# Performance work log

Hardware: AMD Instinct MI355X
Metric: run time of the kernel (lower is better)

The kernel has to match this reference:

```python
import jax, jax.numpy as jnp
import numpy as np

D_MODEL = 1024
N_HEADS = 16
HEAD_DIM = D_MODEL // N_HEADS  # 64
LATENT = 256
B, S = 2, 2048


def setup_inputs() -> dict:
    key = jax.random.key(0)
    ks = jax.random.split(key, 13)
    sc = 0.02
    inp = {
        'x': jax.random.normal(ks[0], (B, S, D_MODEL), jnp.float32),
        'Wq': jax.random.normal(ks[1], (D_MODEL, D_MODEL), jnp.float32) * sc,
        'bq': jnp.zeros((D_MODEL,), jnp.float32),
        'Wkd': jax.random.normal(ks[2], (D_MODEL, LATENT), jnp.float32) * sc,
        'bkd': jnp.zeros((LATENT,), jnp.float32),
        'Wvd': jax.random.normal(ks[3], (D_MODEL, LATENT), jnp.float32) * sc,
        'bvd': jnp.zeros((LATENT,), jnp.float32),
        'Wku': jax.random.normal(ks[4], (LATENT, D_MODEL), jnp.float32) * sc,
        'bku': jnp.zeros((D_MODEL,), jnp.float32),
        'Wvu': jax.random.normal(ks[5], (LATENT, D_MODEL), jnp.float32) * sc,
        'bvu': jnp.zeros((D_MODEL,), jnp.float32),
        'Wo': jax.random.normal(ks[6], (D_MODEL, D_MODEL), jnp.float32) * sc,
        'bo': jnp.zeros((D_MODEL,), jnp.float32),
    }
    return inp


def reference(x, Wq, bq, Wkd, bkd, Wvd, bvd, Wku, bku, Wvu, bvu, Wo, bo):
    b, s, _ = x.shape
    # projections
    Q = x @ Wq + bq                      # [b, s, d_model]
    K_latent = x @ Wkd + bkd             # [b, s, latent]
    V_latent = x @ Wvd + bvd             # [b, s, latent]
    K = K_latent @ Wku + bku             # [b, s, d_model]
    V = V_latent @ Wvu + bvu             # [b, s, d_model]
    # split heads
    Qh = Q.reshape(b, s, N_HEADS, HEAD_DIM)
    Kh = K.reshape(b, s, N_HEADS, HEAD_DIM)
    Vh = V.reshape(b, s, N_HEADS, HEAD_DIM)
    scale = 1.0 / jnp.sqrt(jnp.asarray(HEAD_DIM, x.dtype))
    scores = jnp.einsum('bqhd,bkhd->bhqk', Qh, Kh) * scale  # [b,h,s,s]
    attn = jax.nn.softmax(scores, axis=-1)
    ctx = jnp.einsum('bhqk,bkhd->bqhd', attn, Vh).reshape(b, s, D_MODEL)
    out = ctx @ Wo + bo
    return out
```

## Files before the change

### kernel.cpp

```cpp
#include <hip/hip_runtime.h>
#include <hip/hip_bf16.h>
#include <cstddef>

#define B_SZ 2
#define SEQ  2048
#define DM   1024
#define NH   16
#define HD   64
#define LAT  256
#define MTOT (B_SZ*SEQ)
#define NQKV 1536
#define QSCALE 0.18033688011112042f

typedef short bf16x8 __attribute__((ext_vector_type(8)));
typedef float floatx4 __attribute__((ext_vector_type(4)));
typedef float floatx16 __attribute__((ext_vector_type(16)));
typedef unsigned short u16;

#if __has_builtin(__builtin_amdgcn_exp2f)
#define EXP2(x) __builtin_amdgcn_exp2f(x)
#else
#define EXP2(x) exp2f(x)
#endif

__device__ __forceinline__ u16 f2bf(float f) {
  union { float f; unsigned u; } a; a.f = f;
  unsigned r = a.u + 0x7FFFu + ((a.u >> 16) & 1u);
  return (u16)(r >> 16);
}

__device__ __forceinline__ floatx4 mfma16(bf16x8 a, bf16x8 b, floatx4 c) {
  return __builtin_amdgcn_mfma_f32_16x16x32_bf16(a, b, c, 0, 0, 0);
}

__device__ __forceinline__ floatx16 mfma32(bf16x8 a, bf16x8 b, floatx16 c) {
  return __builtin_amdgcn_mfma_f32_32x32x16_bf16(a, b, c, 0, 0, 0);
}

__device__ __forceinline__ void load16(const u16* g, u16* l) {
  __builtin_amdgcn_global_load_lds((const __attribute__((address_space(1))) unsigned*)g,
                                   (__attribute__((address_space(3))) unsigned*)l, 16, 0, 0);
}

__device__ void transpose_tile(const float* __restrict__ W, u16* __restrict__ WT,
                               int K, int N, int k0, int n0, u16 (*t)[65]) {
  const int r = threadIdx.x >> 4;
  const int c4 = (threadIdx.x & 15) * 4;
#pragma unroll
  for (int s = 0; s < 4; s++) {
    int row = s * 16 + r;
    float4 v = *(const float4*)&W[(size_t)(k0 + row) * N + n0 + c4];
    t[row][c4 + 0] = f2bf(v.x); t[row][c4 + 1] = f2bf(v.y);
    t[row][c4 + 2] = f2bf(v.z); t[row][c4 + 3] = f2bf(v.w);
  }
  __syncthreads();
  const int r2 = threadIdx.x >> 2;
  const int c8 = (threadIdx.x & 3) * 16;
  __align__(16) u16 tmp[16];
#pragma unroll
  for (int i = 0; i < 16; i++) tmp[i] = t[c8 + i][r2];
  u16* dst = WT + (size_t)(n0 + r2) * K + k0 + c8;
  *(bf16x8*)dst       = *(const bf16x8*)&tmp[0];
  *(bf16x8*)(dst + 8) = *(const bf16x8*)&tmp[8];
}

__global__ __launch_bounds__(256)
void prep_k(const float* __restrict__ x, u16* __restrict__ xb,
            const float* __restrict__ Wq, const float* __restrict__ Wkd,
            const float* __restrict__ Wvd, const float* __restrict__ Wku,
            const float* __restrict__ Wvu, const float* __restrict__ Wo,
            u16* __restrict__ WstkT, u16* __restrict__ WkuT,
            u16* __restrict__ WvuT, u16* __restrict__ WoT,
            const float* __restrict__ bq, const float* __restrict__ bkd,
            const float* __restrict__ bvd, float* __restrict__ bqkv) {
  __shared__ u16 t[64][65];
  const int blk = blockIdx.x;
  if (blk < 4096) {
    int i = blk * 256 + threadIdx.x;
    float4 v = ((const float4*)x)[i];
    ushort4 o; o.x = f2bf(v.x); o.y = f2bf(v.y); o.z = f2bf(v.z); o.w = f2bf(v.w);
    ((ushort4*)xb)[i] = o;
  } else if (blk < 4352) {
    int tt = blk - 4096;
    transpose_tile(Wq, WstkT, DM, DM, (tt >> 4) * 64, (tt & 15) * 64, t);
  } else if (blk < 4416) {
    int tt = blk - 4352;
    transpose_tile(Wkd, WstkT + (size_t)DM * DM, DM, LAT, (tt >> 2) * 64, (tt & 3) * 64, t);
  } else if (blk < 4480) {
    int tt = blk - 4416;
    transpose_tile(Wvd, WstkT + (size_t)1280 * DM, DM, LAT, (tt >> 2) * 64, (tt & 3) * 64, t);
  } else if (blk < 4544) {
    int tt = blk - 4480;
    transpose_tile(Wku, WkuT, LAT, DM, (tt >> 4) * 64, (tt & 15) * 64, t);
  } else if (blk < 4608) {
    int tt = blk - 4544;
    transpose_tile(Wvu, WvuT, LAT, DM, (tt >> 4) * 64, (tt & 15) * 64, t);
  } else if (blk < 4864) {
    int tt = blk - 4608;
    transpose_tile(Wo, WoT, DM, DM, (tt >> 4) * 64, (tt & 15) * 64, t);
  } else {
    int i = (blk - 4864) * 256 + threadIdx.x;
    float v = (i < 1024) ? bq[i] : (i < 1280) ? bkd[i - 1024] : bvd[i - 1280];
    bqkv[i] = v;
  }
}

template<int TM, int OUT_BF16, int VT1>
__global__ __launch_bounds__(256)
void gemm_bt(const u16* __restrict__ A0, const u16* __restrict__ A1,
             const u16* __restrict__ BT0, const u16* __restrict__ BT1,
             const float* __restrict__ bias0, const float* __restrict__ bias1,
             void* __restrict__ C0, void* __restrict__ C1,
             int M, int N, int Kd, int lda, float qscale, int qcols) {
  constexpr int FM = TM / 32;
  __shared__ u16 As[TM * 64];
  __shared__ u16 Bs[64 * 64];
  const u16* A  = blockIdx.z ? A1 : A0;
  const u16* BT = blockIdx.z ? BT1 : BT0;
  const float* bias = blockIdx.z ? bias1 : bias0;
  void* C = blockIdx.z ? C1 : C0;

  const int tid = threadIdx.x;
  const int m0 = blockIdx.y * TM, n0 = blockIdx.x * 64;
  const int wave = tid >> 6, lane = tid & 63;
  const int l15 = lane & 15, quad = lane >> 4;
  const int wm = (wave >> 1) * (TM / 2), wn = (wave & 1) * 32;

  floatx4 acc[FM][2];
#pragma unroll
  for (int i = 0; i < FM; i++)
#pragma unroll
    for (int j = 0; j < 2; j++) acc[i][j] = (floatx4){0.f, 0.f, 0.f, 0.f};

  const int tr = tid >> 3;
  const int tc8 = (tid & 7) * 8;
  const u16* Ag = A  + (size_t)(m0 + tr) * lda + tc8;
  const u16* Bg = BT + (size_t)(n0 + tr) * Kd + tc8;
  u16* AsW = &As[(size_t)tid * 8];
  u16* BsW = &Bs[(size_t)tid * 8];

  for (int k0 = 0; k0 < Kd; k0 += 64) {
    __syncthreads();
#pragma unroll
    for (int s = 0; s < FM; s++)
      load16(Ag + (size_t)(s * 32) * lda + k0, AsW + s * 2048);
#pragma unroll
    for (int s = 0; s < 2; s++)
      load16(Bg + (size_t)(s * 32) * Kd  + k0, BsW + s * 2048);
    __syncthreads();
#pragma unroll
    for (int kk = 0; kk < 2; kk++) {
      bf16x8 af[FM], bfr[2];
#pragma unroll
      for (int i = 0; i < FM; i++)
        af[i]  = *(const bf16x8*)&As[(wm + i * 16 + l15) * 64 + kk * 32 + quad * 8];
#pragma unroll
      for (int j = 0; j < 2; j++)
        bfr[j] = *(const bf16x8*)&Bs[(wn + j * 16 + l15) * 64 + kk * 32 + quad * 8];
#pragma unroll
      for (int i = 0; i < FM; i++)
#pragma unroll
        for (int j = 0; j < 2; j++)
          acc[i][j] = mfma16(af[i], bfr[j], acc[i][j]);
    }
  }

  if (VT1 && blockIdx.z == 1) {
#pragma unroll
    for (int i = 0; i < FM; i++) {
      int row = m0 + wm + i * 16 + quad * 4;
      int bb = row >> 11, sb = row & 2047;
#pragma unroll
      for (int j = 0; j < 2; j++) {
        int col = n0 + wn + j * 16 + l15;
        float bv = bias[col];
        union { u16 u[4]; uint2 w2; } tv;
#pragma unroll
        for (int r = 0; r < 4; r++) tv.u[r] = f2bf(acc[i][j][r] + bv);
        *(uint2*)((u16*)C + ((size_t)(bb * 16 + (col >> 6)) * 64 + (col & 63)) * SEQ + sb) = tv.w2;
      }
    }
  } else {
#pragma unroll
    for (int i = 0; i < FM; i++) {
      int row = m0 + wm + i * 16 + quad * 4;
#pragma unroll
      for (int j = 0; j < 2; j++) {
        int col = n0 + wn + j * 16 + l15;
        float bv = bias[col];
        float sc = (col < qcols) ? qscale : 1.f;
#pragma unroll
        for (int r = 0; r < 4; r++) {
          float v = (acc[i][j][r] + bv) * sc;
          if (OUT_BF16) ((u16*)C)[(size_t)(row + r) * N + col] = f2bf(v);
          else          ((float*)C)[(size_t)(row + r) * N + col] = v;
        }
      }
    }
  }
}

__global__ __launch_bounds__(256, 3)
void attn_fused(const u16* __restrict__ Q, const u16* __restrict__ K,
                const u16* __restrict__ VT, u16* __restrict__ CTX) {
  __shared__ __align__(16) u16 KVt[2][2][64][64];
  const int lin = blockIdx.y * gridDim.x + blockIdx.x;
  const int idx = lin >> 3;
  const int bh = (lin & 7) * 4 + (idx >> 4);
  const int q0 = (idx & 15) * 128;
  const int b = bh >> 4, h = bh & 15;
  const int wave = threadIdx.x >> 6, lane = threadIdx.x & 63;
  const int l31 = lane & 31;
  const int hi = lane >> 5;
  const int lr = lane >> 3;
  const int cx = (lane & 7) ^ lr;

  bf16x8 qf[4];
  {
    const u16* Qp = Q + (size_t)(b * SEQ + q0 + wave * 32 + l31) * NQKV + h * HD + hi * 8;
#pragma unroll
    for (int dc = 0; dc < 4; dc++)
      qf[dc] = *(const bf16x8*)(Qp + dc * 16);
  }

  const u16* Ks[2];
  const u16* Vs[2];
#pragma unroll
  for (int s = 0; s < 2; s++) {
    int r = wave * 8 + s * 32 + lr;
    Ks[s] = K + (size_t)(b * SEQ + r) * DM + h * HD + cx * 8;
    Vs[s] = VT + ((size_t)bh * HD + r) * SEQ + cx * 8;
  }

  floatx16 o[2];
  const floatx16 zf16 = {0.f,0.f,0.f,0.f,0.f,0.f,0.f,0.f,0.f,0.f,0.f,0.f,0.f,0.f,0.f,0.f};
  o[0] = zf16; o[1] = zf16;
  float ls = 0.f;

#pragma unroll
  for (int s = 0; s < 2; s++) {
    load16(Ks[s], &KVt[0][0][wave * 8 + s * 32][0]);
    load16(Vs[s], &KVt[0][1][wave * 8 + s * 32][0]);
  }
  __syncthreads();

#pragma unroll 2
  for (int t = 0; t < 32; ++t) {
    const int cur = t & 1, nxt = cur ^ 1;
    if (t < 31) {
      const int kt = (t + 1) * 64;
#pragma unroll
      for (int s = 0; s < 2; s++) {
        load16(Ks[s] + (size_t)kt * DM, &KVt[nxt][0][wave * 8 + s * 32][0]);
        load16(Vs[s] + kt,              &KVt[nxt][1][wave * 8 + s * 32][0]);
      }
    }
#pragma unroll
    for (int kh = 0; kh < 2; kh++) {
      const int rk = kh * 32 + l31;
      bf16x8 kf[4];
#pragma unroll
      for (int dc = 0; dc < 4; dc++)
        kf[dc] = *(const bf16x8*)&KVt[cur][0][rk][((dc * 2 + hi) ^ (rk & 7)) * 8];
      floatx16 z = zf16;
      __builtin_amdgcn_s_setprio(1);
#pragma unroll
      for (int dc = 0; dc < 4; dc++) z = mfma32(kf[dc], qf[dc], z);
      __builtin_amdgcn_s_setprio(0);
      {
        float p0 = EXP2(z[0]), p1 = EXP2(z[1]), p2 = EXP2(z[2]), p3 = EXP2(z[3]);
        float p4 = EXP2(z[4]), p5 = EXP2(z[5]), p6 = EXP2(z[6]), p7 = EXP2(z[7]);
        ls += ((p0 + p1) + (p2 + p3)) + ((p4 + p5) + (p6 + p7));
        unsigned w0 = __builtin_amdgcn_perm(__float_as_uint(p1) + 0x8000u,
                                            __float_as_uint(p0) + 0x8000u, 0x07060302u);
        unsigned w1 = __builtin_amdgcn_perm(__float_as_uint(p3) + 0x8000u,
                                            __float_as_uint(p2) + 0x8000u, 0x07060302u);
        unsigned w2 = __builtin_amdgcn_perm(__float_as_uint(p5) + 0x8000u,
                                            __float_as_uint(p4) + 0x8000u, 0x07060302u);
        unsigned w3 = __builtin_amdgcn_perm(__float_as_uint(p7) + 0x8000u,
                                            __float_as_uint(p6) + 0x8000u, 0x07060302u);
        unsigned s0 = (unsigned)__shfl_xor((int)w0, 32);
        unsigned s1 = (unsigned)__shfl_xor((int)w1, 32);
        unsigned s2 = (unsigned)__shfl_xor((int)w2, 32);
        unsigned s3 = (unsigned)__shfl_xor((int)w3, 32);
        union { unsigned u[4]; bf16x8 v; } b0;
        b0.u[0] = hi ? s2 : w0;
        b0.u[1] = hi ? s3 : w1;
        b0.u[2] = hi ? w2 : s0;
        b0.u[3] = hi ? w3 : s1;
        bf16x8 vf0 = *(const bf16x8*)&KVt[cur][1][l31     ][((kh * 4 + hi) ^ (l31 & 7)) * 8];
        bf16x8 vf1 = *(const bf16x8*)&KVt[cur][1][32 + l31][((kh * 4 + hi) ^ (l31 & 7)) * 8];
        __builtin_amdgcn_s_setprio(1);
        o[0] = mfma32(vf0, b0.v, o[0]);
        o[1] = mfma32(vf1, b0.v, o[1]);
        __builtin_amdgcn_s_setprio(0);
      }
      {
        float p0 = EXP2(z[8]),  p1 = EXP2(z[9]),  p2 = EXP2(z[10]), p3 = EXP2(z[11]);
        float p4 = EXP2(z[12]), p5 = EXP2(z[13]), p6 = EXP2(z[14]), p7 = EXP2(z[15]);
        ls += ((p0 + p1) + (p2 + p3)) + ((p4 + p5) + (p6 + p7));
        unsigned w0 = __builtin_amdgcn_perm(__float_as_uint(p1) + 0x8000u,
                                            __float_as_uint(p0) + 0x8000u, 0x07060302u);
        unsigned w1 = __builtin_amdgcn_perm(__float_as_uint(p3) + 0x8000u,
                                            __float_as_uint(p2) + 0x8000u, 0x07060302u);
        unsigned w2 = __builtin_amdgcn_perm(__float_as_uint(p5) + 0x8000u,
                                            __float_as_uint(p4) + 0x8000u, 0x07060302u);
        unsigned w3 = __builtin_amdgcn_perm(__float_as_uint(p7) + 0x8000u,
                                            __float_as_uint(p6) + 0x8000u, 0x07060302u);
        unsigned s0 = (unsigned)__shfl_xor((int)w0, 32);
        unsigned s1 = (unsigned)__shfl_xor((int)w1, 32);
        unsigned s2 = (unsigned)__shfl_xor((int)w2, 32);
        unsigned s3 = (unsigned)__shfl_xor((int)w3, 32);
        union { unsigned u[4]; bf16x8 v; } b1;
        b1.u[0] = hi ? s2 : w0;
        b1.u[1] = hi ? s3 : w1;
        b1.u[2] = hi ? w2 : s0;
        b1.u[3] = hi ? w3 : s1;
        bf16x8 vf0 = *(const bf16x8*)&KVt[cur][1][l31     ][((kh * 4 + 2 + hi) ^ (l31 & 7)) * 8];
        bf16x8 vf1 = *(const bf16x8*)&KVt[cur][1][32 + l31][((kh * 4 + 2 + hi) ^ (l31 & 7)) * 8];
        __builtin_amdgcn_s_setprio(1);
        o[0] = mfma32(vf0, b1.v, o[0]);
        o[1] = mfma32(vf1, b1.v, o[1]);
        __builtin_amdgcn_s_setprio(0);
      }
    }
    __syncthreads();
  }

  const float lsum = ls + __shfl_xor(ls, 32);
  const float inv = 1.f / lsum;
  u16* Crow = CTX + (size_t)(b * SEQ + q0 + wave * 32 + l31) * DM + h * HD + hi * 4;
#pragma unroll
  for (int dh = 0; dh < 2; dh++)
#pragma unroll
    for (int g = 0; g < 4; g++) {
      union { u16 u[4]; uint2 w2; } tv;
#pragma unroll
      for (int r = 0; r < 4; r++)
        tv.u[r] = f2bf(o[dh][4 * g + r] * inv);
      *(uint2*)(Crow + dh * 32 + g * 8) = tv.w2;
    }
}

extern "C" void kernel_launch(void* const* d_in, const int* in_sizes, int n_in,
                              void* d_out, int out_size, void* d_ws, size_t ws_size,
                              hipStream_t stream) {
  const float* x   = (const float*)d_in[0];
  const float* Wq  = (const float*)d_in[1];
  const float* bq  = (const float*)d_in[2];
  const float* Wkd = (const float*)d_in[3];
  const float* bkd = (const float*)d_in[4];
  const float* Wvd = (const float*)d_in[5];
  const float* bvd = (const float*)d_in[6];
  const float* Wku = (const float*)d_in[7];
  const float* bku = (const float*)d_in[8];
  const float* Wvu = (const float*)d_in[9];
  const float* bvu = (const float*)d_in[10];
  const float* Wo  = (const float*)d_in[11];
  const float* bo  = (const float*)d_in[12];
  float* out = (float*)d_out;

  float* bqkv = (float*)d_ws;
  u16* p = (u16*)((char*)d_ws + 1536 * sizeof(float));
  u16* xb    = p; p += (size_t)MTOT * DM;
  u16* WstkT = p; p += (size_t)NQKV * DM;
  u16* WkuT  = p; p += (size_t)DM * LAT;
  u16* WvuT  = p; p += (size_t)DM * LAT;
  u16* WoT   = p; p += (size_t)DM * DM;
  u16* QKVb  = p; p += (size_t)MTOT * NQKV;
  u16* Kb    = p; p += (size_t)MTOT * DM;
  u16* VTb   = p; p += (size_t)MTOT * DM;
  u16* CXb   = p; p += (size_t)MTOT * DM;

  prep_k<<<4870, 256, 0, stream>>>(x, xb, Wq, Wkd, Wvd, Wku, Wvu, Wo,
                                   WstkT, WkuT, WvuT, WoT, bq, bkd, bvd, bqkv);

  gemm_bt<128, 1, 0><<<dim3(NQKV / 64, MTOT / 128, 1), 256, 0, stream>>>(
      xb, xb, WstkT, WstkT, bqkv, bqkv, QKVb, QKVb, MTOT, NQKV, DM, DM, QSCALE, DM);
  gemm_bt<128, 1, 1><<<dim3(DM / 64, MTOT / 128, 2), 256, 0, stream>>>(
      QKVb + 1024, QKVb + 1280, WkuT, WvuT, bku, bvu, Kb, VTb, MTOT, DM, LAT, NQKV, 1.f, 0);

  attn_fused<<<dim3(SEQ / 128, B_SZ * NH), 256, 0, stream>>>(QKVb, Kb, VTb, CXb);

  gemm_bt<64, 0, 0><<<dim3(DM / 64, MTOT / 64, 1), 256, 0, stream>>>(
      CXb, CXb, WoT, WoT, bo, bo, out, out, MTOT, DM, DM, DM, 1.f, 0);
}
```

Measured before the change: 205.5 us.

## Split key sequence across two wave groups per block in attention

Doubles the attention block to 512 threads, with two groups of four waves each handling half of the key/value sequence for the same 128 queries. Partial outputs and row sums are merged through shared memory at the end. This raises wave-level parallelism and latency hiding per CU. In exchange it doubles LDS use and adds a reduction step, and the tighter launch bound may cause register pressure or spills.

```diff
diff --git a/kernel.cpp b/kernel.cpp
--- a/kernel.cpp
+++ b/kernel.cpp
@@ -200,16 +200,18 @@
   }
 }
 
-__global__ __launch_bounds__(256, 3)
+__global__ __launch_bounds__(512, 3)
 void attn_fused(const u16* __restrict__ Q, const u16* __restrict__ K,
                 const u16* __restrict__ VT, u16* __restrict__ CTX) {
-  __shared__ __align__(16) u16 KVt[2][2][64][64];
+  __shared__ __align__(16) u16 KVt[2][2][2][64][64];
   const int lin = blockIdx.y * gridDim.x + blockIdx.x;
   const int idx = lin >> 3;
   const int bh = (lin & 7) * 4 + (idx >> 4);
   const int q0 = (idx & 15) * 128;
   const int b = bh >> 4, h = bh & 15;
   const int wave = threadIdx.x >> 6, lane = threadIdx.x & 63;
+  const int qw = wave & 3;
+  const int kw = wave >> 2;
   const int l31 = lane & 31;
   const int hi = lane >> 5;
   const int lr = lane >> 3;
@@ -217,7 +219,7 @@
 
   bf16x8 qf[4];
   {
-    const u16* Qp = Q + (size_t)(b * SEQ + q0 + wave * 32 + l31) * NQKV + h * HD + hi * 8;
+    const u16* Qp = Q + (size_t)(b * SEQ + q0 + qw * 32 + l31) * NQKV + h * HD + hi * 8;
 #pragma unroll
     for (int dc = 0; dc < 4; dc++)
       qf[dc] = *(const bf16x8*)(Qp + dc * 16);
@@ -227,9 +229,9 @@
   const u16* Vs[2];
 #pragma unroll
   for (int s = 0; s < 2; s++) {
-    int r = wave * 8 + s * 32 + lr;
-    Ks[s] = K + (size_t)(b * SEQ + r) * DM + h * HD + cx * 8;
-    Vs[s] = VT + ((size_t)bh * HD + r) * SEQ + cx * 8;
+    int r = qw * 8 + s * 32 + lr;
+    Ks[s] = K + (size_t)(b * SEQ + kw * 1024 + r) * DM + h * HD + cx * 8;
+    Vs[s] = VT + ((size_t)bh * HD + r) * SEQ + kw * 1024 + cx * 8;
   }
 
   floatx16 o[2];
@@ -239,20 +241,20 @@
 
 #pragma unroll
   for (int s = 0; s < 2; s++) {
-    load16(Ks[s], &KVt[0][0][wave * 8 + s * 32][0]);
-    load16(Vs[s], &KVt[0][1][wave * 8 + s * 32][0]);
+    load16(Ks[s], &KVt[kw][0][0][qw * 8 + s * 32][0]);
+    load16(Vs[s], &KVt[kw][0][1][qw * 8 + s * 32][0]);
   }
   __syncthreads();
 
 #pragma unroll 2
-  for (int t = 0; t < 32; ++t) {
+  for (int t = 0; t < 16; ++t) {
     const int cur = t & 1, nxt = cur ^ 1;
-    if (t < 31) {
+    if (t < 15) {
       const int kt = (t + 1) * 64;
 #pragma unroll
       for (int s = 0; s < 2; s++) {
-        load16(Ks[s] + (size_t)kt * DM, &KVt[nxt][0][wave * 8 + s * 32][0]);
-        load16(Vs[s] + kt,              &KVt[nxt][1][wave * 8 + s * 32][0]);
+        load16(Ks[s] + (size_t)kt * DM, &KVt[kw][nxt][0][qw * 8 + s * 32][0]);
+        load16(Vs[s] + kt,              &KVt[kw][nxt][1][qw * 8 + s * 32][0]);
       }
     }
 #pragma unroll
@@ -261,7 +263,7 @@
       bf16x8 kf[4];
 #pragma unroll
       for (int dc = 0; dc < 4; dc++)
-        kf[dc] = *(const bf16x8*)&KVt[cur][0][rk][((dc * 2 + hi) ^ (rk & 7)) * 8];
+        kf[dc] = *(const bf16x8*)&KVt[kw][cur][0][rk][((dc * 2 + hi) ^ (rk & 7)) * 8];
       floatx16 z = zf16;
       __builtin_amdgcn_s_setprio(1);
 #pragma unroll
@@ -288,8 +290,8 @@
         b0.u[1] = hi ? s3 : w1;
         b0.u[2] = hi ? w2 : s0;
         b0.u[3] = hi ? w3 : s1;
-        bf16x8 vf0 = *(const bf16x8*)&KVt[cur][1][l31     ][((kh * 4 + hi) ^ (l31 & 7)) * 8];
-        bf16x8 vf1 = *(const bf16x8*)&KVt[cur][1][32 + l31][((kh * 4 + hi) ^ (l31 & 7)) * 8];
+        bf16x8 vf0 = *(const bf16x8*)&KVt[kw][cur][1][l31     ][((kh * 4 + hi) ^ (l31 & 7)) * 8];
+        bf16x8 vf1 = *(const bf16x8*)&KVt[kw][cur][1][32 + l31][((kh * 4 + hi) ^ (l31 & 7)) * 8];
         __builtin_amdgcn_s_setprio(1);
         o[0] = mfma32(vf0, b0.v, o[0]);
         o[1] = mfma32(vf1, b0.v, o[1]);
@@ -316,8 +318,8 @@
         b1.u[1] = hi ? s3 : w1;
         b1.u[2] = hi ? w2 : s0;
         b1.u[3] = hi ? w3 : s1;
-        bf16x8 vf0 = *(const bf16x8*)&KVt[cur][1][l31     ][((kh * 4 + 2 + hi) ^ (l31 & 7)) * 8];
-        bf16x8 vf1 = *(const bf16x8*)&KVt[cur][1][32 + l31][((kh * 4 + 2 + hi) ^ (l31 & 7)) * 8];
+        bf16x8 vf0 = *(const bf16x8*)&KVt[kw][cur][1][l31     ][((kh * 4 + 2 + hi) ^ (l31 & 7)) * 8];
+        bf16x8 vf1 = *(const bf16x8*)&KVt[kw][cur][1][32 + l31][((kh * 4 + 2 + hi) ^ (l31 & 7)) * 8];
         __builtin_amdgcn_s_setprio(1);
         o[0] = mfma32(vf0, b1.v, o[0]);
         o[1] = mfma32(vf1, b1.v, o[1]);
@@ -327,19 +329,36 @@
     __syncthreads();
   }
 
+  float* Osh = (float*)&KVt[0][0][0][0][0];
+  float* Lsh = Osh + 128 * 68;
   const float lsum = ls + __shfl_xor(ls, 32);
-  const float inv = 1.f / lsum;
-  u16* Crow = CTX + (size_t)(b * SEQ + q0 + wave * 32 + l31) * DM + h * HD + hi * 4;
-#pragma unroll
-  for (int dh = 0; dh < 2; dh++)
-#pragma unroll
-    for (int g = 0; g < 4; g++) {
-      union { u16 u[4]; uint2 w2; } tv;
-#pragma unroll
-      for (int r = 0; r < 4; r++)
-        tv.u[r] = f2bf(o[dh][4 * g + r] * inv);
-      *(uint2*)(Crow + dh * 32 + g * 8) = tv.w2;
-    }
+  const int q = qw * 32 + l31;
+  if (kw == 1) {
+#pragma unroll
+    for (int dh = 0; dh < 2; dh++)
+#pragma unroll
+      for (int g = 0; g < 4; g++) {
+        floatx4 tv = {o[dh][4 * g], o[dh][4 * g + 1], o[dh][4 * g + 2], o[dh][4 * g + 3]};
+        *(floatx4*)&Osh[q * 68 + dh * 32 + g * 8 + hi * 4] = tv;
+      }
+    if (hi == 0) Lsh[q] = lsum;
+  }
+  __syncthreads();
+  if (kw == 0) {
+    const float inv = 1.f / (lsum + Lsh[q]);
+    u16* Crow = CTX + (size_t)(b * SEQ + q0 + q) * DM + h * HD + hi * 4;
+#pragma unroll
+    for (int dh = 0; dh < 2; dh++)
+#pragma unroll
+      for (int g = 0; g < 4; g++) {
+        const float* oc = &Osh[q * 68 + dh * 32 + g * 8 + hi * 4];
+        union { u16 u[4]; uint2 w2; } tv;
+#pragma unroll
+        for (int r = 0; r < 4; r++)
+          tv.u[r] = f2bf((o[dh][4 * g + r] + oc[r]) * inv);
+        *(uint2*)(Crow + dh * 32 + g * 8) = tv.w2;
+      }
+  }
 }
 
 extern "C" void kernel_launch(void* const* d_in, const int* in_sizes, int n_in,
@@ -380,7 +399,7 @@
   gemm_bt<128, 1, 1><<<dim3(DM / 64, MTOT / 128, 2), 256, 0, stream>>>(
       QKVb + 1024, QKVb + 1280, WkuT, WvuT, bku, bvu, Kb, VTb, MTOT, DM, LAT, NQKV, 1.f, 0);
 
-  attn_fused<<<dim3(SEQ / 128, B_SZ * NH), 256, 0, stream>>>(QKVb, Kb, VTb, CXb);
+  attn_fused<<<dim3(SEQ / 128, B_SZ * NH), 512, 0, stream>>>(QKVb, Kb, VTb, CXb);
 
   gemm_bt<64, 0, 0><<<dim3(DM / 64, MTOT / 64, 1), 256, 0, stream>>>(
       CXb, CXb, WoT, WoT, bo, bo, out, out, MTOT, DM, DM, DM, 1.f, 0);
```

Result: no change. 207.0 us (+0.7%).
